# Performance work log

Measured on AMD Instinct MI355X. Metric: run time of the kernel, lower is better.

The kernel has to match this reference:

```python
import jax, jax.numpy as jnp
import numpy as np

B, C, H, W = 16, 512, 32, 32
NUM_GROUPS = 32
EPS = 1e-5


def setup_inputs() -> dict:
    key = jax.random.key(0)
    ks = jax.random.split(key, 7)
    x = jax.random.normal(ks[0], (B, C, H, W), dtype=jnp.float32)
    gamma = jnp.ones((C,), dtype=jnp.float32)
    beta = jnp.zeros((C,), dtype=jnp.float32)
    # project_in: Conv2d(C, 3C, 1) -> weight [3C, C], bias [3C]
    w_in = jax.random.normal(ks[1], (3 * C, C), dtype=jnp.float32) / np.sqrt(C)
    b_in = jnp.zeros((3 * C,), dtype=jnp.float32)
    # project_out: Conv2d(C, C, 1) with init_scale=0.0 -> zero-init in original;
    # use small random weights so gradients/outputs are non-trivial for testing.
    w_out = jax.random.normal(ks[2], (C, C), dtype=jnp.float32) / np.sqrt(C)
    b_out = jnp.zeros((C,), dtype=jnp.float32)
    return {"x": x, "gamma": gamma, "beta": beta, "w_in": w_in, "b_in": b_in,
            "w_out": w_out, "b_out": b_out}


def group_norm(x, gamma, beta):
    b, c, h, w = x.shape
    xg = x.reshape(b, NUM_GROUPS, c // NUM_GROUPS, h, w)
    mean = xg.mean(axis=(2, 3, 4), keepdims=True)
    var = xg.var(axis=(2, 3, 4), keepdims=True)
    xn = ((xg - mean) * jax.lax.rsqrt(var + EPS)).reshape(b, c, h, w)
    return xn * gamma[None, :, None, None] + beta[None, :, None, None]


def reference(x, gamma, beta, w_in, b_in, w_out, b_out):
    skip = x  # in_channels == out_channels -> Identity skip
    xn = group_norm(x, gamma, beta)
    # 1x1 conv == channel matmul
    qkv = jnp.einsum('oc,bchw->bohw', w_in, xn) + b_in[None, :, None, None]
    q, k, v = jnp.split(qkv, 3, axis=1)  # each [B, C, H, W]
    cm = q.shape[1]
    # [B, H, W, H*W] scores
    scores = jnp.einsum('bchw,bcHW->bhwHW', q, k).reshape(B, H, W, H * W)
    attn = jax.nn.softmax(scores / jnp.sqrt(jnp.float32(cm)), axis=-1)
    attn = attn.reshape(B, H, W, H, W)
    out = jnp.einsum('bhwHW,bcHW->bchw', attn, v)
    out = jnp.einsum('oc,bchw->bohw', w_out, out) + b_out[None, :, None, None]
    return out + skip
```

## Files before the change

### kernel.cpp

```cpp
#include <hip/hip_runtime.h>
#include <hip/hip_bf16.h>
#include <cstdint>
#include <cstddef>

#define HW   1024
#define NC   512
#define NB   16
#define EPSV 1e-5f

typedef __hip_bfloat16 bf16;
typedef __attribute__((ext_vector_type(8))) __bf16 bf16x8;
typedef __attribute__((ext_vector_type(4))) float f32x4;

__device__ __forceinline__ void gload16(const void* g, void* l) {
  __builtin_amdgcn_global_load_lds(
      (const __attribute__((address_space(1))) uint32_t*)g,
      (__attribute__((address_space(3))) uint32_t*)l, 16, 0, 0);
}

__global__ __launch_bounds__(256) void cvt_w_kernel(
    const float* __restrict__ wi, const float* __restrict__ wo,
    bf16* __restrict__ wib, char* __restrict__ wobf) {
  int i = blockIdx.x * 256 + threadIdx.x;
  if (i < 196608) {
    float4 v = ((const float4*)wi)[i];
    union { bf16 h[4]; uint2 u; } p;
    p.h[0] = __float2bfloat16(v.x); p.h[1] = __float2bfloat16(v.y);
    p.h[2] = __float2bfloat16(v.z); p.h[3] = __float2bfloat16(v.w);
    *(uint2*)&wib[(size_t)i * 4] = p.u;
  } else {
    int j = i - 196608;
    float4 v = ((const float4*)wo)[j];
    int elem = j * 4;
    int co = elem >> 9, c = elem & 511;
    union { bf16 h[4]; uint2 u; } p;
    p.h[0] = __float2bfloat16(v.x); p.h[1] = __float2bfloat16(v.y);
    p.h[2] = __float2bfloat16(v.z); p.h[3] = __float2bfloat16(v.w);
    int chh = co >> 4, col_ = co & 15, kc = c >> 5, cc = c & 31;
    *(uint2*)(wobf + (((chh * 16 + kc) << 10) + col_ * 64 + cc * 2)) = p.u;
  }
}

__global__ __launch_bounds__(256) void gn_kernel(
    const float* __restrict__ x, const float* __restrict__ gamma,
    const float* __restrict__ beta, bf16* __restrict__ xn) {
  int blk = blockIdx.x;
  int b = blk >> 5, g = blk & 31;
  size_t base = ((size_t)(b * NC + g * 16)) * HW;
  const float4* src4 = (const float4*)(x + base);
  int t = threadIdx.x;
  float s = 0.f, ss = 0.f;
  float4 v[16];
#pragma unroll
  for (int i = 0; i < 16; ++i) {
    v[i] = src4[t + i * 256];
    s  += v[i].x + v[i].y + v[i].z + v[i].w;
    ss += v[i].x * v[i].x + v[i].y * v[i].y + v[i].z * v[i].z + v[i].w * v[i].w;
  }
  __shared__ float red[256];
  red[t] = s; __syncthreads();
  for (int o = 128; o > 0; o >>= 1) { if (t < o) red[t] += red[t + o]; __syncthreads(); }
  float mean = red[0] * (1.f / 16384.f);
  __syncthreads();
  red[t] = ss; __syncthreads();
  for (int o = 128; o > 0; o >>= 1) { if (t < o) red[t] += red[t + o]; __syncthreads(); }
  float var = red[0] * (1.f / 16384.f) - mean * mean;
  float rstd = rsqrtf(var + EPSV);

  __shared__ bf16 sm[16][1032];
#pragma unroll
  for (int i = 0; i < 16; ++i) {
    int idx = t + i * 256;
    int c = idx >> 8;
    int hw4 = (idx & 255) * 4;
    float gm = gamma[g * 16 + c], bt = beta[g * 16 + c];
    union { bf16 h[4]; uint2 u; } p;
    p.h[0] = __float2bfloat16((v[i].x - mean) * rstd * gm + bt);
    p.h[1] = __float2bfloat16((v[i].y - mean) * rstd * gm + bt);
    p.h[2] = __float2bfloat16((v[i].z - mean) * rstd * gm + bt);
    p.h[3] = __float2bfloat16((v[i].w - mean) * rstd * gm + bt);
    *(uint2*)&sm[c][hw4] = p.u;
  }
  __syncthreads();
  bf16* dst = xn + (size_t)b * HW * NC + g * 16;
#pragma unroll
  for (int it = 0; it < 8; ++it) {
    int u = it * 256 + t;
    int hw = u >> 1;
    int c8 = (u & 1) * 8;
    union { bf16 h[8]; uint4 q; } p;
#pragma unroll
    for (int j = 0; j < 8; ++j) p.h[j] = sm[c8 + j][hw];
    *(uint4*)&dst[(size_t)hw * NC + c8] = p.q;
  }
}

template <int MODE>
__global__ __launch_bounds__(256) void gemm_bt(
    const bf16* __restrict__ A, int lda, long long sA,
    const bf16* __restrict__ B, int ldb, long long sB,
    void* __restrict__ Cv, int ldc, long long sC,
    int K,
    const float* __restrict__ bias) {
  __shared__ bf16 sT[2][128][32];
  int z = blockIdx.z;
  const bf16* Ab = A + (size_t)z * sA;
  const bf16* Bb = B + (size_t)z * sB;
  int n0 = blockIdx.x * 128, m0 = blockIdx.y * 128;
  int t = threadIdx.x;
  int l = t & 63, w = t >> 6;
  int wm = w >> 1, wn = w & 1;

  int srow = t >> 2;
  int scol = (t & 3) * 8;

  f32x4 acc[4][4] = {};

  const bf16* ga0 = Ab + (size_t)(m0 + srow) * lda + scol;
  const bf16* gb0 = Bb + (size_t)(n0 + srow) * ldb + scol;

  for (int k0 = 0; k0 < K; k0 += 32) {
    gload16(ga0 + k0, &sT[0][srow][scol]);
    gload16(ga0 + (size_t)64 * lda + k0, &sT[0][64 + srow][scol]);
    gload16(gb0 + k0, &sT[1][srow][scol]);
    gload16(gb0 + (size_t)64 * ldb + k0, &sT[1][64 + srow][scol]);
    __syncthreads();
    bf16x8 af[4], bfr[4];
    int kc = (l >> 4) * 8;
    int ra = wm * 64 + (l & 15);
    int rb = wn * 64 + (l & 15);
#pragma unroll
    for (int i = 0; i < 4; ++i) {
      af[i]  = *(const bf16x8*)&sT[0][ra + i * 16][kc];
      bfr[i] = *(const bf16x8*)&sT[1][rb + i * 16][kc];
    }
#pragma unroll
    for (int i = 0; i < 4; ++i)
#pragma unroll
      for (int j = 0; j < 4; ++j)
        acc[i][j] = __builtin_amdgcn_mfma_f32_16x16x32_bf16(af[i], bfr[j], acc[i][j], 0, 0, 0);
    __syncthreads();
  }

  int rbase = (l >> 4) * 4;
#pragma unroll
  for (int i = 0; i < 4; ++i) {
    int row = m0 + wm * 64 + i * 16 + rbase;
    float4 bv = *(const float4*)&bias[row];
    float bb[4] = {bv.x, bv.y, bv.z, bv.w};
#pragma unroll
    for (int j = 0; j < 4; ++j) {
      int col = n0 + wn * 64 + j * 16 + (l & 15);
      if (MODE == 0) {
        bf16* C = (bf16*)Cv + (size_t)z * sC;
        union { bf16 h[4]; uint2 u; } p;
#pragma unroll
        for (int r = 0; r < 4; ++r) p.h[r] = __float2bfloat16(acc[i][j][r] + bb[r]);
        *(uint2*)&C[(size_t)col * ldc + row] = p.u;
      } else if (MODE == 4) {
        char* C = (char*)Cv + (size_t)z * sC * 2;
        int tile = col >> 7, jgc = (col >> 4) & 7, j_lo = col & 15;
        int kw = row >> 5, cc = row & 31;
        union { bf16 h[4]; uint2 u; } p;
#pragma unroll
        for (int r = 0; r < 4; ++r) p.h[r] = __float2bfloat16(acc[i][j][r] + bb[r]);
        *(uint2*)(C + (((tile * 8 + jgc) * 16 + kw) << 10) + j_lo * 64 + cc * 2) = p.u;
      } else {
        char* C = (char*)Cv + (size_t)z * sC * 2;
        int tile = col >> 7, jj = col & 127;
        int ks = jj >> 5, jc = jj & 31;
#pragma unroll
        for (int r = 0; r < 4; ++r) {
          int ch = row + r;
          int chh = ch >> 4, chl = ch & 15;
          *(bf16*)(C + (((tile * 32 + chh) * 4 + ks) << 10)
                     + chl * 64 + jc * 2) = __float2bfloat16(acc[i][j][r] + bb[r]);
        }
      }
    }
  }
}

__global__ __launch_bounds__(512, 1) void flash_kernel(
    const bf16* __restrict__ qtok, const bf16* __restrict__ kfrag,
    const bf16* __restrict__ vfrag, const bf16* __restrict__ wfrag,
    const float* __restrict__ b_out, const float* __restrict__ x,
    float* __restrict__ out) {
  __shared__ char lds[98304];
  char* Qs = lds;
  char* Ps = lds + 65536;
  float* redl = (float*)(lds + 65536);

  int id = blockIdx.x;
  int xcd = id & 7, rest = id >> 3;
  int q = rest & 15, bh = rest >> 4;
  int b = xcd + bh * 8;
  int i0 = q * 64;

  const char* qC = (const char*)qtok + (size_t)b * 1048576;
  const char* kC = (const char*)kfrag + (size_t)b * 1048576;
  const char* vC = (const char*)vfrag + (size_t)b * 1048576;
  const char* wC = (const char*)wfrag;

  int t = threadIdx.x, l = t & 63, w = t >> 6;
  int l15 = l & 15, lq = l >> 4;
  int fofs = l15 * 64 + lq * 16;
  int chb = w * 64;

#pragma unroll
  for (int it = 0; it < 8; ++it) {
    int A = it * 8192 + t * 16;
    int ih2 = A >> 14, ks = (A >> 10) & 15, ilo = (A >> 6) & 15, cb = A & 63;
    gload16(qC + (size_t)(i0 + ih2 * 16 + ilo) * 1024 + ks * 64 + cb, Qs + A);
  }

  float lacc[4] = {0.f, 0.f, 0.f, 0.f};
  f32x4 o[4][4] = {};
  const float scl = 0.044194173824159216f;

  __syncthreads();

  for (int tile = 0; tile < 8; ++tile) {
    char* Pc = Ps + (tile & 1) * 16384;
    bf16x8 vf[4][4];
#pragma unroll
    for (int ks = 0; ks < 4; ++ks)
#pragma unroll
      for (int mi = 0; mi < 4; ++mi)
        vf[ks][mi] = *(const bf16x8*)(vC
            + (((size_t)(tile * 32 + (w * 4 + mi)) * 4 + ks) << 10) + fofs);
    f32x4 s[4] = {};
#pragma unroll
    for (int kw = 0; kw < 16; ++kw) {
      bf16x8 kf = *(const bf16x8*)(kC
          + (((size_t)(tile * 8 + w) * 16 + kw) << 10) + fofs);
#pragma unroll
      for (int ni = 0; ni < 4; ++ni) {
        bf16x8 qf = *(const bf16x8*)(Qs + ni * 16384 + kw * 1024 + fofs);
        s[ni] = __builtin_amdgcn_mfma_f32_16x16x32_bf16(kf, qf, s[ni], 0, 0, 0);
      }
    }
#pragma unroll
    for (int ni = 0; ni < 4; ++ni) {
      float p0 = __expf(s[ni][0] * scl);
      float p1 = __expf(s[ni][1] * scl);
      float p2 = __expf(s[ni][2] * scl);
      float p3 = __expf(s[ni][3] * scl);
      lacc[ni] += p0 + p1 + p2 + p3;
      union { bf16 h[4]; uint64_t u; } pk;
      pk.h[0] = __float2bfloat16(p0); pk.h[1] = __float2bfloat16(p1);
      pk.h[2] = __float2bfloat16(p2); pk.h[3] = __float2bfloat16(p3);
      *(uint64_t*)(Pc + ni * 4096 + (w >> 1) * 1024 + l15 * 64
                   + (w & 1) * 32 + lq * 8) = pk.u;
    }
    __syncthreads();
#pragma unroll
    for (int ks = 0; ks < 4; ++ks)
#pragma unroll
      for (int ni = 0; ni < 4; ++ni) {
        bf16x8 pf = *(const bf16x8*)(Pc + ni * 4096 + ks * 1024 + fofs);
#pragma unroll
        for (int mi = 0; mi < 4; ++mi)
          o[mi][ni] = __builtin_amdgcn_mfma_f32_16x16x32_bf16(vf[ks][mi], pf, o[mi][ni], 0, 0, 0);
      }
  }

#pragma unroll
  for (int ni = 0; ni < 4; ++ni) {
    float v = lacc[ni];
    v += __shfl_xor(v, 16);
    v += __shfl_xor(v, 32);
    if (l < 16) redl[w * 64 + ni * 16 + l] = v;
  }
  __syncthreads();
  float linv[4];
#pragma unroll
  for (int ni = 0; ni < 4; ++ni) {
    int i = ni * 16 + l15;
    float v = redl[i];
#pragma unroll
    for (int w2 = 1; w2 < 8; ++w2) v += redl[w2 * 64 + i];
    linv[ni] = 1.f / v;
  }
#pragma unroll
  for (int mi = 0; mi < 4; ++mi)
#pragma unroll
    for (int ni = 0; ni < 4; ++ni) {
      union { bf16 h[4]; uint64_t u; } pk;
#pragma unroll
      for (int r = 0; r < 4; ++r)
        pk.h[r] = __float2bfloat16(o[mi][ni][r] * linv[ni]);
      int dst = ni * 16384 + (w * 2 + (mi >> 1)) * 1024 + l15 * 64
              + (mi & 1) * 32 + lq * 8;
      *(uint64_t*)(Qs + dst) = pk.u;
    }
  __syncthreads();

  f32x4 acc2[4][4] = {};
#pragma unroll
  for (int kc = 0; kc < 16; ++kc) {
    bf16x8 wf[4];
#pragma unroll
    for (int mi = 0; mi < 4; ++mi)
      wf[mi] = *(const bf16x8*)(wC + (((size_t)(w * 4 + mi) * 16 + kc) << 10) + fofs);
#pragma unroll
    for (int ni = 0; ni < 4; ++ni) {
      bf16x8 pf = *(const bf16x8*)(Qs + ni * 16384 + kc * 1024 + fofs);
#pragma unroll
      for (int mi = 0; mi < 4; ++mi)
        acc2[mi][ni] = __builtin_amdgcn_mfma_f32_16x16x32_bf16(wf[mi], pf, acc2[mi][ni], 0, 0, 0);
    }
  }

  const float* xb = x + (size_t)b * 524288;
  float* ob = out + (size_t)b * 524288;
#pragma unroll
  for (int mi = 0; mi < 4; ++mi) {
    int cbase = chb + mi * 16 + lq * 4;
    float4 bv = *(const float4*)&b_out[cbase];
    float bb[4] = {bv.x, bv.y, bv.z, bv.w};
#pragma unroll
    for (int ni = 0; ni < 4; ++ni) {
      int i = i0 + ni * 16 + l15;
#pragma unroll
      for (int r = 0; r < 4; ++r) {
        size_t off = (size_t)(cbase + r) * 1024 + i;
        ob[off] = acc2[mi][ni][r] + bb[r] + xb[off];
      }
    }
  }
}

extern "C" void kernel_launch(void* const* d_in, const int* in_sizes, int n_in,
                              void* d_out, int out_size, void* d_ws, size_t ws_size,
                              hipStream_t stream) {
  const float* x     = (const float*)d_in[0];
  const float* gamma = (const float*)d_in[1];
  const float* beta  = (const float*)d_in[2];
  const float* w_in  = (const float*)d_in[3];
  const float* b_in  = (const float*)d_in[4];
  const float* w_out = (const float*)d_in[5];
  const float* b_out = (const float*)d_in[6];
  float* out = (float*)d_out;

  char* w = (char*)d_ws;
  bf16* xn    = (bf16*)w;
  bf16* qtok  = (bf16*)(w + ((size_t)16 << 20));
  bf16* kfrag = (bf16*)(w + ((size_t)32 << 20));
  bf16* vfrag = (bf16*)(w + ((size_t)48 << 20));
  bf16* wib   = (bf16*)(w + ((size_t)64 << 20));
  char* wobf  = (char*)(w + ((size_t)64 << 20) + ((size_t)3 << 19));

  cvt_w_kernel<<<1024, 256, 0, stream>>>(w_in, w_out, wib, wobf);
  gn_kernel<<<NB * 32, 256, 0, stream>>>(x, gamma, beta, xn);

  gemm_bt<0><<<dim3(8, 4, NB), 256, 0, stream>>>(
      wib, 512, 0, xn, 512, 512 * 1024, qtok, 512, 512 * 1024, 512, b_in);
  gemm_bt<4><<<dim3(8, 4, NB), 256, 0, stream>>>(
      wib + 512 * 512, 512, 0, xn, 512, 512 * 1024, kfrag, 0, 512 * 1024, 512,
      b_in + 512);
  gemm_bt<5><<<dim3(8, 4, NB), 256, 0, stream>>>(
      wib + 1024 * 512, 512, 0, xn, 512, 512 * 1024, vfrag, 0, 512 * 1024, 512,
      b_in + 1024);

  flash_kernel<<<256, 512, 0, stream>>>(qtok, kfrag, vfrag, (const bf16*)wobf,
                                        b_out, x, out);
}
```

Measured before the change: 142.9 us.

## Double key tile width per iteration in flash attention kernel

Each flash-attention loop iteration now covers 256 keys instead of 128, so there are 4 iterations instead of 8. Each wave computes two 16-key score fragments that share the same Q fragment loads from LDS, and the PV phase loads V fragments in two halves. The K-fragment output layout of the projection GEMM is flattened to match the new indexing. This halves the number of barrier-separated iterations and reuses Q reads, at the cost of more registers, the loss of P double-buffering (a second barrier per iteration), and possible occupancy or spill pressure.

New measurement: 137.2 us. 4.0% less time.

```diff
diff --git a/kernel.cpp b/kernel.cpp
--- a/kernel.cpp
+++ b/kernel.cpp
@@ -159,12 +159,12 @@
         *(uint2*)&C[(size_t)col * ldc + row] = p.u;
       } else if (MODE == 4) {
         char* C = (char*)Cv + (size_t)z * sC * 2;
-        int tile = col >> 7, jgc = (col >> 4) & 7, j_lo = col & 15;
+        int jflat = col >> 4, j_lo = col & 15;
         int kw = row >> 5, cc = row & 31;
         union { bf16 h[4]; uint2 u; } p;
 #pragma unroll
         for (int r = 0; r < 4; ++r) p.h[r] = __float2bfloat16(acc[i][j][r] + bb[r]);
-        *(uint2*)(C + (((tile * 8 + jgc) * 16 + kw) << 10) + j_lo * 64 + cc * 2) = p.u;
+        *(uint2*)(C + (((size_t)(jflat * 16 + kw)) << 10) + j_lo * 64 + cc * 2) = p.u;
       } else {
         char* C = (char*)Cv + (size_t)z * sC * 2;
         int tile = col >> 7, jj = col & 127;
@@ -220,49 +220,74 @@
 
   __syncthreads();
 
-  for (int tile = 0; tile < 8; ++tile) {
-    char* Pc = Ps + (tile & 1) * 16384;
-    bf16x8 vf[4][4];
-#pragma unroll
-    for (int ks = 0; ks < 4; ++ks)
-#pragma unroll
-      for (int mi = 0; mi < 4; ++mi)
-        vf[ks][mi] = *(const bf16x8*)(vC
-            + (((size_t)(tile * 32 + (w * 4 + mi)) * 4 + ks) << 10) + fofs);
-    f32x4 s[4] = {};
+  for (int tile = 0; tile < 4; ++tile) {
+    bf16x8 vfA[4][4];
+#pragma unroll
+    for (int js = 0; js < 4; ++js)
+#pragma unroll
+      for (int mi = 0; mi < 4; ++mi) {
+        int f = tile * 8 + js;
+        vfA[js][mi] = *(const bf16x8*)(vC
+            + (((size_t)(((f >> 2) * 32 + (w * 4 + mi)) * 4 + (f & 3))) << 10) + fofs);
+      }
+    f32x4 s0[4] = {}, s1[4] = {};
 #pragma unroll
     for (int kw = 0; kw < 16; ++kw) {
-      bf16x8 kf = *(const bf16x8*)(kC
-          + (((size_t)(tile * 8 + w) * 16 + kw) << 10) + fofs);
+      int jf0 = tile * 16 + w * 2;
+      bf16x8 kf0 = *(const bf16x8*)(kC + (((size_t)(jf0 * 16 + kw)) << 10) + fofs);
+      bf16x8 kf1 = *(const bf16x8*)(kC + (((size_t)((jf0 + 1) * 16 + kw)) << 10) + fofs);
 #pragma unroll
       for (int ni = 0; ni < 4; ++ni) {
         bf16x8 qf = *(const bf16x8*)(Qs + ni * 16384 + kw * 1024 + fofs);
-        s[ni] = __builtin_amdgcn_mfma_f32_16x16x32_bf16(kf, qf, s[ni], 0, 0, 0);
+        s0[ni] = __builtin_amdgcn_mfma_f32_16x16x32_bf16(kf0, qf, s0[ni], 0, 0, 0);
+        s1[ni] = __builtin_amdgcn_mfma_f32_16x16x32_bf16(kf1, qf, s1[ni], 0, 0, 0);
       }
     }
 #pragma unroll
     for (int ni = 0; ni < 4; ++ni) {
-      float p0 = __expf(s[ni][0] * scl);
-      float p1 = __expf(s[ni][1] * scl);
-      float p2 = __expf(s[ni][2] * scl);
-      float p3 = __expf(s[ni][3] * scl);
-      lacc[ni] += p0 + p1 + p2 + p3;
-      union { bf16 h[4]; uint64_t u; } pk;
-      pk.h[0] = __float2bfloat16(p0); pk.h[1] = __float2bfloat16(p1);
-      pk.h[2] = __float2bfloat16(p2); pk.h[3] = __float2bfloat16(p3);
-      *(uint64_t*)(Pc + ni * 4096 + (w >> 1) * 1024 + l15 * 64
-                   + (w & 1) * 32 + lq * 8) = pk.u;
+#pragma unroll
+      for (int jg = 0; jg < 2; ++jg) {
+        const f32x4& sv = jg ? s1[ni] : s0[ni];
+        float p0 = __expf(sv[0] * scl);
+        float p1 = __expf(sv[1] * scl);
+        float p2 = __expf(sv[2] * scl);
+        float p3 = __expf(sv[3] * scl);
+        lacc[ni] += p0 + p1 + p2 + p3;
+        union { bf16 h[4]; uint64_t u; } pk;
+        pk.h[0] = __float2bfloat16(p0); pk.h[1] = __float2bfloat16(p1);
+        pk.h[2] = __float2bfloat16(p2); pk.h[3] = __float2bfloat16(p3);
+        *(uint64_t*)(Ps + ni * 8192 + w * 1024 + l15 * 64 + jg * 32 + lq * 8) = pk.u;
+      }
     }
     __syncthreads();
-#pragma unroll
-    for (int ks = 0; ks < 4; ++ks)
+    bf16x8 vfB[4][4];
+#pragma unroll
+    for (int js = 0; js < 4; ++js)
+#pragma unroll
+      for (int mi = 0; mi < 4; ++mi) {
+        int f = tile * 8 + 4 + js;
+        vfB[js][mi] = *(const bf16x8*)(vC
+            + (((size_t)(((f >> 2) * 32 + (w * 4 + mi)) * 4 + (f & 3))) << 10) + fofs);
+      }
+#pragma unroll
+    for (int js = 0; js < 4; ++js)
 #pragma unroll
       for (int ni = 0; ni < 4; ++ni) {
-        bf16x8 pf = *(const bf16x8*)(Pc + ni * 4096 + ks * 1024 + fofs);
+        bf16x8 pf = *(const bf16x8*)(Ps + ni * 8192 + js * 1024 + fofs);
 #pragma unroll
         for (int mi = 0; mi < 4; ++mi)
-          o[mi][ni] = __builtin_amdgcn_mfma_f32_16x16x32_bf16(vf[ks][mi], pf, o[mi][ni], 0, 0, 0);
-      }
+          o[mi][ni] = __builtin_amdgcn_mfma_f32_16x16x32_bf16(vfA[js][mi], pf, o[mi][ni], 0, 0, 0);
+      }
+#pragma unroll
+    for (int js = 0; js < 4; ++js)
+#pragma unroll
+      for (int ni = 0; ni < 4; ++ni) {
+        bf16x8 pf = *(const bf16x8*)(Ps + ni * 8192 + (4 + js) * 1024 + fofs);
+#pragma unroll
+        for (int mi = 0; mi < 4; ++mi)
+          o[mi][ni] = __builtin_amdgcn_mfma_f32_16x16x32_bf16(vfB[js][mi], pf, o[mi][ni], 0, 0, 0);
+      }
+    __syncthreads();
   }
 
 #pragma unroll
```
